# Kernel tuning notes

Hardware: AMD Instinct MI355X
Metric: run time of the kernel (lower is better)

Reference implementation:

```python
import jax
import jax.numpy as jnp
import numpy as np
from jax import lax
from jax.scipy.special import logsumexp

B, T, D = 8, 512, 768
S, H, O = 8, 32, 32
TRANS_W, EMISS_W = 0.5, 0.5


def setup_inputs() -> dict:
    key = jax.random.key(0)
    ks = jax.random.split(key, 8)
    emb = jax.random.normal(ks[0], (B, T, D), dtype=jnp.float32)
    u = jax.random.uniform(ks[1], (B, T, S, O), minval=1e-3, maxval=1.0)
    obs = (u / u.sum(-1, keepdims=True)).astype(jnp.float32)
    seq_lengths = jax.random.randint(ks[2], (B,), T // 2, T + 1).at[0].set(T).astype(jnp.int32)
    # HMM params (match torch init)
    priors = jnp.zeros(H).at[0].set(1.0) + jnp.full(H, 0.001).at[0].set(0.0)
    priors = jnp.full(H, 0.001).at[0].set(1.0)
    state_priors = jnp.log(priors)
    unnorm_trans = jax.random.normal(ks[3], (H, H))
    unnorm_emiss = jnp.zeros((S, H, O))
    # xavier_uniform with relu gain
    gain = np.sqrt(2.0)
    a_t = gain * np.sqrt(6.0 / (D + H * H))
    Wt = jax.random.uniform(ks[4], (D, H * H), minval=-a_t, maxval=a_t)
    bt = jnp.zeros(H * H)
    a_e = gain * np.sqrt(6.0 / (D + H * O))
    We = jax.random.uniform(ks[5], (S, D, H * O), minval=-a_e, maxval=a_e)
    be = jnp.zeros((S, H * O))
    return {"emb": emb, "obs": obs, "seq_lengths": seq_lengths,
            "state_priors": state_priors, "unnorm_trans": unnorm_trans,
            "unnorm_emiss": unnorm_emiss, "Wt": Wt, "bt": bt, "We": We, "be": be}


def _chmm_forward(emb, obs, state_priors, unnorm_trans, unnorm_emiss, Wt, bt, We, be, seq_lengths):
    b, t, d = emb.shape
    s, h, o = unnorm_emiss.shape
    lsp = jax.nn.log_softmax(state_priors)                               # [H]
    trans = jax.nn.softmax(unnorm_trans, axis=-1)                        # [H,H]
    emiss = jax.nn.softmax(unnorm_emiss, axis=-1)                        # [S,H,O]
    nn_trans = jax.nn.softmax((emb @ Wt + bt).reshape(b, t, h, h), axis=-1)
    nn_emiss = jax.nn.softmax((jnp.einsum('btd,sde->btse', emb, We) + be).reshape(b, t, s, h, o), axis=-1)
    log_trans = jnp.log((1.0 - TRANS_W) * trans + TRANS_W * nn_trans)    # [B,T,H,H]
    log_emiss = jnp.log((1.0 - EMISS_W) * emiss + EMISS_W * nn_emiss)    # [B,T,S,H,O]

    # normalize_observation: replace non-observing sources on entity positions
    lbs = jnp.argmax(obs, axis=-1)                                       # [B,T,S]
    entity = lbs.sum(-1) > 0                                             # [B,T]
    no_ent = lbs == 0                                                    # [B,T,S]
    mask = entity[:, :, None] & no_ent
    subst = jnp.full((o,), 0.99 / o).at[0].set(0.01)
    obs = jnp.where(mask[..., None], subst, obs)

    # log emission probs: logsumexp over obs dim, sum over sources -> [B,T,H]
    lep = logsumexp(log_emiss + jnp.log(obs)[:, :, :, None, :], axis=-1).sum(axis=2)

    # forward recursion (normalized alpha), scan over time
    a0 = lsp + lep[:, 0]
    a0 = a0 - logsumexp(a0, axis=-1, keepdims=True)
    lep_t = jnp.swapaxes(lep, 0, 1)          # [T,B,H]
    tr_t = jnp.swapaxes(log_trans, 0, 1)     # [T,B,H,H]

    def fstep(a, x):
        lep_i, tr_i = x
        la = lep_i + logsumexp(a[:, :, None] + tr_i, axis=1)
        la = la - logsumexp(la, axis=-1, keepdims=True)
        return la, la

    _, alphas = lax.scan(fstep, a0, (lep_t[1:], tr_t[1:]))
    log_alpha = jnp.swapaxes(jnp.concatenate([a0[None], alphas], 0), 0, 1)   # [B,T,H]

    # backward recursion (reverse scan); uses lep at time t (faithful to source)
    def bstep(bv, x):
        lep_i, tr_i = x
        nb = logsumexp(tr_i + (lep_i + bv)[:, None, :], axis=-1)
        return nb, nb

    _, betas = lax.scan(bstep, jnp.zeros((b, h)), (lep_t[:-1], tr_t[:-1]), reverse=True)
    log_beta = jnp.swapaxes(jnp.concatenate([betas, jnp.zeros((1, b, h))], 0), 0, 1)  # [B,T,H]
    shifts = seq_lengths - t
    log_beta = jax.vmap(lambda bb, ss: jnp.roll(bb, ss, axis=0))(log_beta, shifts)

    log_gamma = log_alpha + log_beta
    ng = log_gamma - logsumexp(log_gamma, axis=-1, keepdims=True)
    # xi for t = 1..T-1 (vectorized, no recursion)
    xi = log_trans[:, 1:] + log_alpha[:, :-1, :, None] + (lep[:, 1:] + log_beta[:, 1:])[:, :, None, :]
    xi = xi - logsumexp(xi.reshape(b, t - 1, -1), axis=-1)[..., None, None]

    log_prior = (jnp.exp(ng[:, 0]) * lsp).sum(-1).mean()
    tran_terms = (jnp.exp(xi) * log_trans[:, 1:]).sum((-2, -1))          # [B,T-1]
    t1 = jnp.arange(t - 1)[None, :]
    log_tran = jnp.where(t1 < (seq_lengths - 1)[:, None], tran_terms, 0.0).sum(-1).mean()
    emis_terms = (jnp.exp(ng) * lep).sum(-1)                             # [B,T]
    t2 = jnp.arange(t)[None, :]
    log_emis = jnp.where(t2 < seq_lengths[:, None], emis_terms, 0.0).sum(-1).mean()
    ll = log_prior + log_tran + log_emis
    return ll, log_trans, log_emiss


def reference(emb, obs, seq_lengths, state_priors, unnorm_trans, unnorm_emiss, Wt, bt, We, be):
    return _chmm_forward(emb, obs, state_priors, unnorm_trans, unnorm_emiss, Wt, bt, We, be, seq_lengths)
```

## Files before the change

kernel.cpp:

```cpp
#include <hip/hip_runtime.h>
#include <hip/hip_bf16.h>


typedef __attribute__((ext_vector_type(8))) short bf16x8;
typedef __attribute__((ext_vector_type(4))) float f32x4;

#define B_M     0
#define B_LDOT  16777216
#define B_CHNK  16777216
#define B_ABND  18874368
#define B_BBND  18907136
#define B_PART  18939904
#define B_LEP   20971520
#define B_ELEP  21496064
#define B_ALIN  22020352
#define B_BLIN  22544640
#define B_TRSM  23068928
#define B_EMSM  23073024
#define B_OBSM  23105792
#define B_ABF   27447552
#define B_WTBF  33739008

#define OUT_TR_BASE 1
#define OUT_EM_BASE 4194305

__device__ __forceinline__ float wsum32(float v) {
#pragma unroll
  for (int m = 16; m >= 1; m >>= 1) v += __shfl_xor(v, m);
  return v;
}
__device__ __forceinline__ float wmax32(float v) {
#pragma unroll
  for (int m = 16; m >= 1; m >>= 1) v = fmaxf(v, __shfl_xor(v, m));
  return v;
}
__device__ __forceinline__ short f2bf(float f) {
  union { float f; unsigned int u; } c; c.f = f;
  unsigned int u = c.u;
  unsigned int r = (u + 0x7FFFu + ((u >> 16) & 1u)) >> 16;
  return (short)r;
}
__device__ __forceinline__ void gload16(const void* g, void* l) {
  __builtin_amdgcn_global_load_lds(
      (const __attribute__((address_space(1))) unsigned int*)g,
      (__attribute__((address_space(3))) unsigned int*)l, 16, 0, 0);
}

__global__ __launch_bounds__(256) void k_prep(
    const float* __restrict__ emb, short* __restrict__ Abf,
    const float* __restrict__ Wt, const float* __restrict__ We,
    short* __restrict__ WT,
    const float* __restrict__ ut, const float* __restrict__ ue,
    float* __restrict__ tsm, float* __restrict__ esm,
    const float* __restrict__ obs, float* __restrict__ om) {
  __shared__ float tile[32][33];
  __shared__ int lbs_s[8];
  __shared__ int entf;
  const int blk = blockIdx.x;
  const int tid = threadIdx.x;
  if (blk < 3072) {
    const int idx = (blk * 256 + tid) * 4;
#pragma unroll
    for (int c = 0; c < 4; ++c) Abf[idx + c] = f2bf(emb[idx + c]);
  } else if (blk < 9984) {
    const int x = blk - 3072;
    const int nb = (x % 288) * 32, kb = (x / 288) * 32;
    const int tx = tid & 31, ty = tid >> 5;
#pragma unroll
    for (int ii = 0; ii < 4; ++ii) {
      const int k = kb + ty + ii * 8;
      const int n = nb + tx;
      float v;
      if (n < 1024) v = Wt[(size_t)k * 1024 + n];
      else {
        const int ne = n - 1024, s = ne >> 10, c = ne & 1023;
        v = We[((size_t)s * 768 + k) * 1024 + c];
      }
      tile[ty + ii * 8][tx] = v;
    }
    __syncthreads();
#pragma unroll
    for (int ii = 0; ii < 4; ++ii) {
      const int n = nb + ty + ii * 8;
      const int k = kb + tx;
      WT[(size_t)n * 768 + k] = f2bf(tile[tx][ty + ii * 8]);
    }
  } else if (blk < 14080) {
    const int bt = blk - 9984;
    const int o = tid & 31;
    const float v = obs[((size_t)bt << 8) + tid];
    float bv = v; int am = o;
#pragma unroll
    for (int m = 16; m >= 1; m >>= 1) {
      const float ov_ = __shfl_xor(bv, m);
      const int oa = __shfl_xor(am, m);
      if (ov_ > bv || (ov_ == bv && oa < am)) { bv = ov_; am = oa; }
    }
    if (o == 0) lbs_s[tid >> 5] = am;
    __syncthreads();
    if (tid == 0) {
      int e = 0;
#pragma unroll
      for (int s = 0; s < 8; ++s) e += lbs_s[s];
      entf = (e > 0) ? 1 : 0;
    }
    __syncthreads();
    const bool msk = entf && (lbs_s[tid >> 5] == 0);
    const float sub = (o == 0) ? 0.01f : (0.99f / 32.0f);
    om[((size_t)bt << 8) + tid] = msk ? sub : v;
  } else {
    const int row = (blk - 14080) * 8 + (tid >> 5);
    const int j = tid & 31;
    const float* src; float* dst;
    if (row < 32) { src = ut + row * 32; dst = tsm + row * 32; }
    else          { src = ue + (row - 32) * 32; dst = esm + (row - 32) * 32; }
    float v = src[j];
    float mx = wmax32(v);
    float e = __expf(v - mx);
    float s = wsum32(e);
    dst[j] = e / s;
  }
}

#define BM 128
#define BN 128
#define BK 64

__global__ __launch_bounds__(512, 4) void gemm_epi(
    const short* __restrict__ A, const short* __restrict__ WT,
    const float* __restrict__ btb, const float* __restrict__ beb,
    const float* __restrict__ tsm, const float* __restrict__ esm,
    const float* __restrict__ om,
    float* __restrict__ out, float* __restrict__ wsM, float* __restrict__ ldot) {
  __shared__ __align__(16) char smem[32768];
  short* lsA = (short*)smem;
  short* lsB = (short*)(smem + 16384);
  float* lsOm = (float*)smem;

  const int bid = blockIdx.x;
  const int xcd = bid & 7;
  const int local = bid >> 3;
  const int ntile = xcd * 9 + (local % 9);
  const int mtile = local / 9;
  const int m0 = mtile * BM;
  const int n0 = ntile * BN;

  const int tid = threadIdx.x;
  const int lane = tid & 63;
  const int w = tid >> 6;
  const int wr = w >> 1, wc = w & 1;
  const int l15 = lane & 15, lq = lane >> 4;

  const int lr = lane >> 3;
  const int lc = (lane & 7) ^ lr;
  const short* gA = A + (size_t)(m0 + (w << 3) + lr) * 768 + (lc << 3);
  const short* gB = WT + (size_t)(n0 + (w << 3) + lr) * 768 + (lc << 3);
  const int lofs = (w << 10) + (lane << 4);
  char* lA = (char*)lsA + lofs;
  char* lB = (char*)lsB + lofs;

  f32x4 acc[2][4] = {};

  for (int kt = 0; kt < 768; kt += BK) {
#pragma unroll
    for (int it = 0; it < 2; ++it) {
      gload16(gA + it * (64 * 768) + kt, lA + (it << 13));
      gload16(gB + it * (64 * 768) + kt, lB + (it << 13));
    }
    __syncthreads();
#pragma unroll
    for (int kk = 0; kk < 2; ++kk) {
      const int kbyte = kk * 64 + lq * 16;
      bf16x8 af[2], bfr[4];
#pragma unroll
      for (int mi = 0; mi < 2; ++mi) {
        const int m = wr * 32 + mi * 16 + l15;
        af[mi] = *(const bf16x8*)((const char*)lsA + ((m * 128 + kbyte) ^ ((m & 7) << 4)));
      }
#pragma unroll
      for (int ni = 0; ni < 4; ++ni) {
        const int n = wc * 64 + ni * 16 + l15;
        bfr[ni] = *(const bf16x8*)((const char*)lsB + ((n * 128 + kbyte) ^ ((n & 7) << 4)));
      }
#pragma unroll
      for (int mi = 0; mi < 2; ++mi)
#pragma unroll
        for (int ni = 0; ni < 4; ++ni)
          acc[mi][ni] = __builtin_amdgcn_mfma_f32_16x16x32_bf16(af[mi], bfr[ni], acc[mi][ni], 0, 0, 0);
    }
    __syncthreads();
  }

  const bool isem = (n0 >= 1024);
  int sblk = 0;
  if (isem) {
    sblk = (n0 - 1024) >> 10;
    const int row = tid >> 2, part = (tid & 3) << 3;
    const float* src = om + (((size_t)(m0 + row)) << 8) + (sblk << 5) + part;
    float* dst = lsOm + row * 36 + part;
    *(float4*)dst = *(const float4*)src;
    *(float4*)(dst + 4) = *(const float4*)(src + 4);
    __syncthreads();
  }

#pragma unroll
  for (int g = 0; g < 2; ++g) {
    const int nbase = n0 + wc * 64 + g * 32;
    const int c0 = nbase + l15;
    const int c1 = c0 + 16;
    const float bias0 = isem ? beb[c0 - 1024] : btb[c0];
    const float bias1 = isem ? beb[c1 - 1024] : btb[c1];
    const float base0 = isem ? esm[c0 - 1024] : tsm[c0];
    const float base1 = isem ? esm[c1 - 1024] : tsm[c1];
    const int h = (nbase >> 5) & 31;
#pragma unroll
    for (int mi = 0; mi < 2; ++mi) {
      const int rl0 = wr * 32 + mi * 16 + lq * 4;
      const int rowb = m0 + rl0;
      float e0[4], e1[4], sm[4];
#pragma unroll
      for (int r = 0; r < 4; ++r) {
        e0[r] = __expf(acc[mi][2 * g][r] + bias0);
        e1[r] = __expf(acc[mi][2 * g + 1][r] + bias1);
        sm[r] = e0[r] + e1[r];
      }
#pragma unroll
      for (int m_ = 1; m_ < 16; m_ <<= 1) {
#pragma unroll
        for (int r = 0; r < 4; ++r) sm[r] += __shfl_xor(sm[r], m_);
      }
      float M0[4], M1[4], lg0[4], lg1[4];
#pragma unroll
      for (int r = 0; r < 4; ++r) {
        const float inv = 0.5f * __builtin_amdgcn_rcpf(sm[r]);
        M0[r] = 0.5f * base0 + e0[r] * inv;
        M1[r] = 0.5f * base1 + e1[r] * inv;
        lg0[r] = __logf(M0[r]);
        lg1[r] = __logf(M1[r]);
      }
      if (!isem) {
#pragma unroll
        for (int r = 0; r < 4; ++r) {
          const size_t rb = ((size_t)(rowb + r)) << 10;
          out[OUT_TR_BASE + rb + c0] = lg0[r];
          out[OUT_TR_BASE + rb + c1] = lg1[r];
          wsM[rb + c0] = M0[r];
          wsM[rb + c1] = M1[r];
        }
      } else {
        const int ne0 = c0 - 1024;
        float dt[4];
#pragma unroll
        for (int r = 0; r < 4; ++r) {
          const float* ov = lsOm + (rl0 + r) * 36;
          dt[r] = M0[r] * ov[l15] + M1[r] * ov[l15 + 16];
        }
#pragma unroll
        for (int m_ = 1; m_ < 16; m_ <<= 1) {
#pragma unroll
          for (int r = 0; r < 4; ++r) dt[r] += __shfl_xor(dt[r], m_);
        }
#pragma unroll
        for (int r = 0; r < 4; ++r) {
          const size_t rb = ((size_t)(rowb + r)) << 13;
          out[OUT_EM_BASE + rb + ne0] = lg0[r];
          out[OUT_EM_BASE + rb + ne0 + 16] = lg1[r];
        }
        if (l15 == 0) {
#pragma unroll
          for (int r = 0; r < 4; ++r)
            ldot[(((size_t)(rowb + r)) << 8) + (sblk << 5) + h] = __logf(dt[r]);
        }
      }
    }
  }
}

__global__ __launch_bounds__(64) void k_elep(const float* __restrict__ ldot,
                                             float* __restrict__ lep,
                                             float* __restrict__ elep) {
  const int bt = blockIdx.x;
  const int l = threadIdx.x, i = l & 31;
  const float* ld = ldot + ((size_t)bt << 8);
  float v = 0.f;
#pragma unroll
  for (int s = 0; s < 8; ++s) v += ld[(s << 5) + i];
  float mx = wmax32(v);
  if (l < 32) {
    lep[((size_t)bt << 5) + i] = v;
    elep[((size_t)bt << 5) + i] = __expf(v - mx);
  }
}

__global__ __launch_bounds__(256) void k_chunk(const float* __restrict__ M,
                                               const float* __restrict__ elep,
                                               float* __restrict__ chnk) {
  const int blk = blockIdx.x;
  const int dir = blk >> 8;
  const int b = (blk >> 5) & 7, c = blk & 31;
  int t0, t1;
  if (dir == 0) { t0 = 16 * c + 1; t1 = 16 * c + 16; if (t1 > 511) t1 = 511; }
  else          { t0 = 16 * c;     t1 = 16 * c + 15; if (t1 > 510) t1 = 510; }
  const size_t base = (size_t)b << 9;
  __shared__ float Pl[1024];
  __shared__ float Gl[1024];
  __shared__ float red[4];
  const int tid = threadIdx.x;
  const int r = tid >> 3;
  const int cq = (tid & 7) << 2;
  float4 p;
  {
    const float4 m = *(const float4*)(M + ((base + t0) << 10) + (tid << 2));
    const float4 e = *(const float4*)(elep + ((base + t0) << 5) + cq);
    p.x = m.x * e.x; p.y = m.y * e.y; p.z = m.z * e.z; p.w = m.w * e.w;
  }
  for (int t = t0 + 1; t <= t1; ++t) {
    *(float4*)(Pl + (tid << 2)) = p;
    const float4 m = *(const float4*)(M + ((base + t) << 10) + (tid << 2));
    const float4 e = *(const float4*)(elep + ((base + t) << 5) + cq);
    float4 g;
    g.x = m.x * e.x; g.y = m.y * e.y; g.z = m.z * e.z; g.w = m.w * e.w;
    *(float4*)(Gl + (tid << 2)) = g;
    __syncthreads();
    float4 nv = {0.f, 0.f, 0.f, 0.f};
#pragma unroll
    for (int j = 0; j < 32; ++j) {
      const float pr = Pl[(r << 5) + j];
      const float4 gj = *(const float4*)(Gl + (j << 5) + cq);
      nv.x = fmaf(pr, gj.x, nv.x);
      nv.y = fmaf(pr, gj.y, nv.y);
      nv.z = fmaf(pr, gj.z, nv.z);
      nv.w = fmaf(pr, gj.w, nv.w);
    }
    float mx = fmaxf(fmaxf(nv.x, nv.y), fmaxf(nv.z, nv.w));
#pragma unroll
    for (int mm = 32; mm >= 1; mm >>= 1) mx = fmaxf(mx, __shfl_xor(mx, mm));
    if ((tid & 63) == 0) red[tid >> 6] = mx;
    __syncthreads();
    mx = fmaxf(fmaxf(red[0], red[1]), fmaxf(red[2], red[3]));
    const float rs = __builtin_amdgcn_rcpf(mx);
    p.x = nv.x * rs; p.y = nv.y * rs; p.z = nv.z * rs; p.w = nv.w * rs;
  }
  *(float4*)(chnk + ((size_t)blk << 10) + (tid << 2)) = p;
}

__global__ __launch_bounds__(64) void k_stitch(const float* __restrict__ chnk,
                                               const float* __restrict__ elep,
                                               const float* __restrict__ sp,
                                               float* __restrict__ ab,
                                               float* __restrict__ bb) {
  const int l = threadIdx.x, i = l & 31, half = l >> 5;
  const int bid = blockIdx.x;
  const int b = bid & 7;
  float v;
  float pb0[16], pb1[16];
  if (bid < 8) {
    const float* base = chnk + ((size_t)(b << 5) << 10);
    auto LDP = [&](float (&pb)[16], int c) {
      const float* P = base + ((size_t)c << 10) + ((half << 4) << 5) + i;
#pragma unroll
      for (int jj = 0; jj < 16; ++jj) pb[jj] = P[jj << 5];
    };
    auto STEP = [&](float (&pb)[16], int c) {
      float pj[16];
#pragma unroll
      for (int jj = 0; jj < 16; ++jj) pj[jj] = __shfl(v, (half << 4) + jj);
      float a0 = 0.f, a1 = 0.f, a2 = 0.f, a3 = 0.f;
#pragma unroll
      for (int q = 0; q < 4; ++q) {
        a0 = fmaf(pj[(q << 2) + 0], pb[(q << 2) + 0], a0);
        a1 = fmaf(pj[(q << 2) + 1], pb[(q << 2) + 1], a1);
        a2 = fmaf(pj[(q << 2) + 2], pb[(q << 2) + 2], a2);
        a3 = fmaf(pj[(q << 2) + 3], pb[(q << 2) + 3], a3);
      }
      float av = (a0 + a1) + (a2 + a3);
      av += __shfl_xor(av, 32);
      const float S = wsum32(av);
      v = av * __builtin_amdgcn_rcpf(S);
      if (l < 32) ab[(((b << 5) + (c + 1)) << 5) + i] = v;
    };
    {
      float u = sp[i];
      float mx = wmax32(u);
      float pe = __expf(u - mx);
      float s = wsum32(pe);
      v = (pe / s) * elep[((size_t)(b << 9) << 5) + i];
      float S = wsum32(v);
      v /= S;
      if (l < 32) ab[((b << 5) << 5) + i] = v;
    }
    LDP(pb0, 0);
    int c = 0;
    for (; c + 1 <= 30; c += 2) {
      LDP(pb1, c + 1);
      STEP(pb0, c);
      LDP(pb0, (c + 2 <= 30) ? c + 2 : 30);
      STEP(pb1, c + 1);
    }
    if (c == 30) STEP(pb0, 30);
  } else {
    const float* base = chnk + ((size_t)(256 + (b << 5)) << 10);
    auto LDP = [&](float (&pb)[16], int c) {
      const float4* P = (const float4*)(base + ((size_t)c << 10) + (i << 5) + (half << 4));
#pragma unroll
      for (int q = 0; q < 4; ++q) {
        const float4 x = P[q];
        pb[(q << 2) + 0] = x.x; pb[(q << 2) + 1] = x.y;
        pb[(q << 2) + 2] = x.z; pb[(q << 2) + 3] = x.w;
      }
    };
    auto STEP = [&](float (&pb)[16], int c) {
      float qj[16];
#pragma unroll
      for (int jj = 0; jj < 16; ++jj) qj[jj] = __shfl(v, (half << 4) + jj);
      float a0 = 0.f, a1 = 0.f, a2 = 0.f, a3 = 0.f;
#pragma unroll
      for (int q = 0; q < 4; ++q) {
        a0 = fmaf(qj[(q << 2) + 0], pb[(q << 2) + 0], a0);
        a1 = fmaf(qj[(q << 2) + 1], pb[(q << 2) + 1], a1);
        a2 = fmaf(qj[(q << 2) + 2], pb[(q << 2) + 2], a2);
        a3 = fmaf(qj[(q << 2) + 3], pb[(q << 2) + 3], a3);
      }
      float av = (a0 + a1) + (a2 + a3);
      av += __shfl_xor(av, 32);
      const float S = wsum32(av);
      v = av * __builtin_amdgcn_rcpf(S);
      if (l < 32) bb[(((b << 5) + c) << 5) + i] = v;
    };
    v = 1.0f / 32.0f;
    LDP(pb0, 31);
    int c = 31;
    for (; c - 1 >= 1; c -= 2) {
      LDP(pb1, c - 1);
      STEP(pb0, c);
      LDP(pb0, (c - 2 >= 1) ? c - 2 : 1);
      STEP(pb1, c - 1);
    }
    if (c == 1) STEP(pb0, 1);
  }
}

__global__ __launch_bounds__(64) void k_recon(const float* __restrict__ M,
                                              const float* __restrict__ elep,
                                              const float* __restrict__ ab,
                                              const float* __restrict__ bb,
                                              float* __restrict__ alin,
                                              float* __restrict__ blin) {
  const int l = threadIdx.x, i = l & 31, half = l >> 5;
  const int blk = blockIdx.x;
  const int dir = blk >> 8;
  const int b = (blk >> 5) & 7, c = blk & 31;
  const size_t base = (size_t)b << 9;
  const float* Mb = M + (base << 10);
  const float* Eb = elep + (base << 5);
  float v;
  float m0[16], m1[16];
  float e0, e1;
  if (dir == 0) {
    float* Ab = alin + (base << 5);
    const int cb = ((half << 4) << 5) + i;
    auto LDF = [&](float (&mb)[16], float& eb, int t) {
      const float* Mr = Mb + ((size_t)t << 10) + cb;
#pragma unroll
      for (int jj = 0; jj < 16; ++jj) mb[jj] = Mr[jj << 5];
      eb = Eb[(t << 5) + i];
    };
    auto STEPF = [&](float (&mb)[16], float eb, int t) {
      float pj[16];
#pragma unroll
      for (int jj = 0; jj < 16; ++jj) pj[jj] = __shfl(v, (half << 4) + jj);
      float a0 = 0.f, a1 = 0.f, a2 = 0.f, a3 = 0.f;
#pragma unroll
      for (int q = 0; q < 4; ++q) {
        a0 = fmaf(pj[(q << 2) + 0], mb[(q << 2) + 0], a0);
        a1 = fmaf(pj[(q << 2) + 1], mb[(q << 2) + 1], a1);
        a2 = fmaf(pj[(q << 2) + 2], mb[(q << 2) + 2], a2);
        a3 = fmaf(pj[(q << 2) + 3], mb[(q << 2) + 3], a3);
      }
      float av = (a0 + a1) + (a2 + a3);
      av += __shfl_xor(av, 32);
      const float nv = av * eb;
      const float S = wsum32(nv);
      v = nv * __builtin_amdgcn_rcpf(S);
      if (l < 32) Ab[(t << 5) + i] = v;
    };
    v = ab[(((b << 5) + c) << 5) + i];
    const int t0 = c << 4;
    if (l < 32) Ab[(t0 << 5) + i] = v;
    const int te = t0 + 15;
    LDF(m0, e0, t0 + 1);
    int t = t0 + 1;
    for (; t + 1 <= te; t += 2) {
      LDF(m1, e1, t + 1);
      STEPF(m0, e0, t);
      LDF(m0, e0, (t + 2 <= te) ? t + 2 : te);
      STEPF(m1, e1, t + 1);
    }
    if (t == te) STEPF(m0, e0, t);
  } else {
    float* Bb = blin + (base << 5);
    auto LDB = [&](float (&mb)[16], float& eb, int t) {
      const float4* Mr = (const float4*)(Mb + ((size_t)t << 10) + (i << 5) + (half << 4));
#pragma unroll
      for (int q = 0; q < 4; ++q) {
        const float4 x = Mr[q];
        mb[(q << 2) + 0] = x.x; mb[(q << 2) + 1] = x.y;
        mb[(q << 2) + 2] = x.z; mb[(q << 2) + 3] = x.w;
      }
      eb = Eb[(t << 5) + i];
    };
    auto STEPB = [&](float (&mb)[16], float eb, int t) {
      const float q0 = v * eb;
      float qj[16];
#pragma unroll
      for (int jj = 0; jj < 16; ++jj) qj[jj] = __shfl(q0, (half << 4) + jj);
      float a0 = 0.f, a1 = 0.f, a2 = 0.f, a3 = 0.f;
#pragma unroll
      for (int q = 0; q < 4; ++q) {
        a0 = fmaf(qj[(q << 2) + 0], mb[(q << 2) + 0], a0);
        a1 = fmaf(qj[(q << 2) + 1], mb[(q << 2) + 1], a1);
        a2 = fmaf(qj[(q << 2) + 2], mb[(q << 2) + 2], a2);
        a3 = fmaf(qj[(q << 2) + 3], mb[(q << 2) + 3], a3);
      }
      float av = (a0 + a1) + (a2 + a3);
      av += __shfl_xor(av, 32);
      const float S = wsum32(av);
      v = av * __builtin_amdgcn_rcpf(S);
      if (l < 32) Bb[(t << 5) + i] = v;
    };
    int ts;
    if (c == 31) {
      v = 1.0f / 32.0f;
      if (l < 32) Bb[(511 << 5) + i] = v;
      ts = 510;
    } else {
      v = bb[(((b << 5) + (c + 1)) << 5) + i];
      ts = (c << 4) + 15;
    }
    const int te = c << 4;
    LDB(m0, e0, ts);
    int t = ts;
    for (; t - 1 >= te; t -= 2) {
      LDB(m1, e1, t - 1);
      STEPB(m0, e0, t);
      LDB(m0, e0, (t - 2 >= te) ? t - 2 : te);
      STEPB(m1, e1, t - 1);
    }
    if (t == te) STEPB(m0, e0, t);
  }
}

__global__ __launch_bounds__(64) void k_final(
    const float* __restrict__ out_log,
    const float* __restrict__ alin, const float* __restrict__ blin,
    const float* __restrict__ elep, const float* __restrict__ lep,
    const int* __restrict__ seqlen, const float* __restrict__ sp,
    float* __restrict__ part) {
  const int bt = blockIdx.x;
  const int b = bt >> 9, t = bt & 511;
  const int l = threadIdx.x, i = l & 31;
  const int L = seqlen[b];
  const int tb = (t + 512 - L) & 511;
  const float a = alin[((size_t)bt << 5) + i];
  const float br = blin[((((size_t)b << 9) + tb) << 5) + i];
  const float g = a * br;
  float Z = wsum32(g);
  Z = fmaxf(Z, 1e-37f);
  const float ng = g / Z;
  const float es = wsum32(ng * lep[((size_t)bt << 5) + i]);
  float pr = 0.0f;
  if (t == 0) {
    const float v = sp[i];
    const float mx = wmax32(v);
    const float pe = __expf(v - mx);
    const float ss = wsum32(pe);
    const float lsp = v - mx - __logf(ss);
    pr = wsum32(ng * lsp);
  }
  float tran = 0.0f;
  if (t >= 1) {
    const float u = elep[((size_t)bt << 5) + i] * br;
    const int jb = (l & 1) << 4;
    float uj[16];
#pragma unroll
    for (int jj = 0; jj < 16; ++jj) uj[jj] = __shfl(u, jb + jj);
    const float ap = alin[(((size_t)bt - 1) << 5) + (l >> 1)];
    const float* Lr = out_log + OUT_TR_BASE + ((size_t)bt << 10) + ((l >> 1) << 5) + jb;
    float accZ = 0.0f, accT = 0.0f;
#pragma unroll
    for (int c = 0; c < 16; ++c) {
      const float lv = Lr[c];
      const float wv = __expf(lv) * ap * uj[c];
      accZ += wv;
      accT = fmaf(wv, lv, accT);
    }
#pragma unroll
    for (int m_ = 32; m_ >= 1; m_ >>= 1) {
      accZ += __shfl_xor(accZ, m_);
      accT += __shfl_xor(accT, m_);
    }
    tran = accT / accZ;
  }
  if (l == 0) {
    part[bt * 3 + 0] = (t == 0) ? pr : 0.0f;
    part[bt * 3 + 1] = (t >= 1 && t < L) ? tran : 0.0f;
    part[bt * 3 + 2] = (t < L) ? es : 0.0f;
  }
}

__global__ __launch_bounds__(256) void k_ll(const float* __restrict__ part,
                                            float* __restrict__ out) {
  __shared__ float red[8];
  const int tid = threadIdx.x;
  const int b = tid >> 5, i = tid & 31;
  float s = 0.0f;
#pragma unroll
  for (int k = 0; k < 16; ++k) {
    const int bt = (b << 9) + (k << 5) + i;
    s += part[bt * 3 + 0] + part[bt * 3 + 1] + part[bt * 3 + 2];
  }
  s = wsum32(s);
  if (i == 0) red[b] = s;
  __syncthreads();
  if (tid == 0) {
    float v = 0.0f;
#pragma unroll
    for (int b2 = 0; b2 < 8; ++b2) v += red[b2];
    out[0] = v / 8.0f;
  }
}

extern "C" void kernel_launch(void* const* d_in, const int* in_sizes, int n_in,
                              void* d_out, int out_size, void* d_ws, size_t ws_size,
                              hipStream_t stream) {
  const float* emb    = (const float*)d_in[0];
  const float* obs    = (const float*)d_in[1];
  const int*   seqlen = (const int*)  d_in[2];
  const float* sp     = (const float*)d_in[3];
  const float* utr    = (const float*)d_in[4];
  const float* uem    = (const float*)d_in[5];
  const float* Wt     = (const float*)d_in[6];
  const float* btb    = (const float*)d_in[7];
  const float* We     = (const float*)d_in[8];
  const float* beb    = (const float*)d_in[9];
  float* out = (float*)d_out;
  char* ws = (char*)d_ws;

  float* wsM  = (float*)(ws + B_M);
  float* ldot = (float*)(ws + B_LDOT);
  float* chnk = (float*)(ws + B_CHNK);
  float* abnd = (float*)(ws + B_ABND);
  float* bbnd = (float*)(ws + B_BBND);
  float* part = (float*)(ws + B_PART);
  float* lep  = (float*)(ws + B_LEP);
  float* elep = (float*)(ws + B_ELEP);
  float* alin = (float*)(ws + B_ALIN);
  float* blin = (float*)(ws + B_BLIN);
  float* tsm  = (float*)(ws + B_TRSM);
  float* esm  = (float*)(ws + B_EMSM);
  float* om   = (float*)(ws + B_OBSM);
  short* Abf  = (short*)(ws + B_ABF);
  short* WTbf = (short*)(ws + B_WTBF);

  k_prep<<<14116, 256, 0, stream>>>(emb, Abf, Wt, We, WTbf, utr, uem, tsm, esm,
                                    obs, om);
  gemm_epi<<<2304, 512, 0, stream>>>(Abf, WTbf, btb, beb, tsm, esm, om,
                                     out, wsM, ldot);
  k_elep<<<4096, 64, 0, stream>>>(ldot, lep, elep);
  k_chunk<<<512, 256, 0, stream>>>(wsM, elep, chnk);
  k_stitch<<<16, 64, 0, stream>>>(chnk, elep, sp, abnd, bbnd);
  k_recon<<<512, 64, 0, stream>>>(wsM, elep, abnd, bbnd, alin, blin);
  k_final<<<4096, 64, 0, stream>>>(out, alin, blin, elep, lep, seqlen, sp, part);
  k_ll<<<1, 256, 0, stream>>>(part, out);
}
```

Measured before the change: 165.0 us.

## Triple-buffer GEMM LDS tiles with async prefetch and halved K-step

Replaces the single-buffered BK=64 load/sync/compute loop with a three-stage LDS ring of BK=32 tiles. Global-to-LDS loads run two stages ahead, and completion is tracked with explicit vmcnt waits and one barrier per iteration. The goal is to overlap global memory latency with MFMA work and remove one of the two barriers per K step. In exchange, LDS use grows to 48KB, which may limit occupancy, and each iteration does less MFMA work.

```diff
diff --git a/kernel.cpp b/kernel.cpp
--- a/kernel.cpp
+++ b/kernel.cpp
@@ -124,7 +124,7 @@
 
 #define BM 128
 #define BN 128
-#define BK 64
+#define BK 32
 
 __global__ __launch_bounds__(512, 4) void gemm_epi(
     const short* __restrict__ A, const short* __restrict__ WT,
@@ -132,9 +132,7 @@
     const float* __restrict__ tsm, const float* __restrict__ esm,
     const float* __restrict__ om,
     float* __restrict__ out, float* __restrict__ wsM, float* __restrict__ ldot) {
-  __shared__ __align__(16) char smem[32768];
-  short* lsA = (short*)smem;
-  short* lsB = (short*)(smem + 16384);
+  __shared__ __align__(16) char smem[49152];
   float* lsOm = (float*)smem;
 
   const int bid = blockIdx.x;
@@ -151,44 +149,54 @@
   const int wr = w >> 1, wc = w & 1;
   const int l15 = lane & 15, lq = lane >> 4;
 
-  const int lr = lane >> 3;
-  const int lc = (lane & 7) ^ lr;
-  const short* gA = A + (size_t)(m0 + (w << 3) + lr) * 768 + (lc << 3);
-  const short* gB = WT + (size_t)(n0 + (w << 3) + lr) * 768 + (lc << 3);
+  const int srow = (w << 4) + (lane >> 2);
+  const int lc = (lane & 3) ^ ((lane >> 2) & 3);
+  const short* gA = A + (size_t)(m0 + srow) * 768 + (lc << 3);
+  const short* gB = WT + (size_t)(n0 + srow) * 768 + (lc << 3);
   const int lofs = (w << 10) + (lane << 4);
-  char* lA = (char*)lsA + lofs;
-  char* lB = (char*)lsB + lofs;
 
   f32x4 acc[2][4] = {};
 
-  for (int kt = 0; kt < 768; kt += BK) {
-#pragma unroll
-    for (int it = 0; it < 2; ++it) {
-      gload16(gA + it * (64 * 768) + kt, lA + (it << 13));
-      gload16(gB + it * (64 * 768) + kt, lB + (it << 13));
-    }
-    __syncthreads();
-#pragma unroll
-    for (int kk = 0; kk < 2; ++kk) {
-      const int kbyte = kk * 64 + lq * 16;
-      bf16x8 af[2], bfr[4];
-#pragma unroll
-      for (int mi = 0; mi < 2; ++mi) {
-        const int m = wr * 32 + mi * 16 + l15;
-        af[mi] = *(const bf16x8*)((const char*)lsA + ((m * 128 + kbyte) ^ ((m & 7) << 4)));
-      }
-#pragma unroll
-      for (int ni = 0; ni < 4; ++ni) {
-        const int n = wc * 64 + ni * 16 + l15;
-        bfr[ni] = *(const bf16x8*)((const char*)lsB + ((n * 128 + kbyte) ^ ((n & 7) << 4)));
-      }
-#pragma unroll
-      for (int mi = 0; mi < 2; ++mi)
-#pragma unroll
-        for (int ni = 0; ni < 4; ++ni)
-          acc[mi][ni] = __builtin_amdgcn_mfma_f32_16x16x32_bf16(af[mi], bfr[ni], acc[mi][ni], 0, 0, 0);
-    }
-    __syncthreads();
+  auto STAGE = [&](int bi, int kt) {
+    char* dA = smem + (bi << 14) + lofs;
+    gload16(gA + kt, dA);
+    gload16(gB + kt, dA + 8192);
+  };
+
+  STAGE(0, 0);
+  STAGE(1, 32);
+  asm volatile("s_waitcnt vmcnt(2)" ::: "memory");
+  __builtin_amdgcn_s_barrier();
+  __builtin_amdgcn_sched_barrier(0);
+
+  int b0 = 0, b1 = 1, b2 = 2;
+#pragma unroll 3
+  for (int it = 0; it < 24; ++it) {
+    if (it < 22) STAGE(b2, (it + 2) * 32);
+    const char* sA = smem + (b0 << 14);
+    const char* sB = sA + 8192;
+    bf16x8 af[2], bfr[4];
+#pragma unroll
+    for (int mi = 0; mi < 2; ++mi) {
+      const int m = wr * 32 + mi * 16 + l15;
+      af[mi] = *(const bf16x8*)(sA + (m << 6) + ((lq ^ (m & 3)) << 4));
+    }
+#pragma unroll
+    for (int ni = 0; ni < 4; ++ni) {
+      const int n = wc * 64 + ni * 16 + l15;
+      bfr[ni] = *(const bf16x8*)(sB + (n << 6) + ((lq ^ (n & 3)) << 4));
+    }
+#pragma unroll
+    for (int mi = 0; mi < 2; ++mi)
+#pragma unroll
+      for (int ni = 0; ni < 4; ++ni)
+        acc[mi][ni] = __builtin_amdgcn_mfma_f32_16x16x32_bf16(af[mi], bfr[ni], acc[mi][ni], 0, 0, 0);
+    if (it < 22)      asm volatile("s_waitcnt vmcnt(2)" ::: "memory");
+    else if (it < 23) asm volatile("s_waitcnt vmcnt(0)" ::: "memory");
+    __builtin_amdgcn_sched_barrier(0);
+    __builtin_amdgcn_s_barrier();
+    __builtin_amdgcn_sched_barrier(0);
+    const int tb = b0; b0 = b1; b1 = b2; b2 = tb;
   }
 
   const bool isem = (n0 >= 1024);
```

Measured after the change: 171.5 us (median of 2 runs). 3.9% more time.
